# Kernel optimization log

Measured on AMD Instinct MI355X. Metric: run time of the kernel, lower is better.

Reference implementation:

```python
import jax, jax.numpy as jnp
import numpy as np

B, S, N = 1, 512, 256
C_M, C_Z, C_OPM, C_H, H = 64, 128, 32, 32, 8
INF = 1.0e6


def layer_norm(x, w, b, eps=1e-5):
    mu = x.mean(-1, keepdims=True)
    var = x.var(-1, keepdims=True)
    return (x - mu) / jnp.sqrt(var + eps) * w + b


def setup_inputs() -> dict:
    key = jax.random.key(0)
    ks = jax.random.split(key, 12)
    inp = {
        'm': jax.random.normal(ks[0], (B, S, N, C_M), jnp.float32),
        'z': jax.random.normal(ks[1], (B, N, N, C_Z), jnp.float32),
        'msa_mask': jnp.ones((B, S, N), jnp.float32),
        'pair_mask': jnp.ones((B, N, N), jnp.float32),
        # OuterProductMean params
        'opm_norm_w': jnp.ones((C_M,), jnp.float32),
        'opm_norm_b': jnp.zeros((C_M,), jnp.float32),
        'opm_a_w': jax.random.normal(ks[2], (C_OPM, C_M), jnp.float32) * 0.05,
        'opm_b_w': jax.random.normal(ks[3], (C_OPM, C_M), jnp.float32) * 0.05,
        'opm_o_w': jax.random.normal(ks[4], (C_Z, C_OPM * C_OPM), jnp.float32) * 0.02,
        'opm_o_b': jnp.zeros((C_Z,), jnp.float32),
        # PairWeightedAveraging params
        'pwa_norm_m_w': jnp.ones((C_M,), jnp.float32),
        'pwa_norm_m_b': jnp.zeros((C_M,), jnp.float32),
        'pwa_norm_z_w': jnp.ones((C_Z,), jnp.float32),
        'pwa_norm_z_b': jnp.zeros((C_Z,), jnp.float32),
        'pwa_m_w': jax.random.normal(ks[5], (H * C_H, C_M), jnp.float32) * 0.05,
        'pwa_g_w': jax.random.normal(ks[6], (H * C_H, C_M), jnp.float32) * 0.05,
        'pwa_z_w': jax.random.normal(ks[7], (H, C_Z), jnp.float32) * 0.05,
        'pwa_o_w': jax.random.normal(ks[8], (C_M, H * C_H), jnp.float32) * 0.02,
    }
    return inp


def reference(m, z, msa_mask, pair_mask,
              opm_norm_w, opm_norm_b, opm_a_w, opm_b_w, opm_o_w, opm_o_b,
              pwa_norm_m_w, pwa_norm_m_b, pwa_norm_z_w, pwa_norm_z_b,
              pwa_m_w, pwa_g_w, pwa_z_w, pwa_o_w):
    # ---- OuterProductMean: m (B,S,N,c_in), msa_mask (B,S,N) -> (B,N,N,c_z)
    mn = layer_norm(m, opm_norm_w, opm_norm_b)
    a = jnp.einsum('bsni,ci->bsnc', mn, opm_a_w) * msa_mask[..., None]  # (B,S,N,c)
    bb = jnp.einsum('bsni,ci->bsnc', mn, opm_b_w) * msa_mask[..., None]
    num_mask = jnp.clip(jnp.einsum('bsi,bsj->bij', msa_mask, msa_mask), 1.0)
    # outer product mean over S; flatten (c,d) with c-major to match torch reshape
    zt = jnp.einsum('bsic,bsjd->bijcd', a, bb).reshape(B, N, N, C_OPM * C_OPM)
    zt = zt / num_mask[..., None]
    z_opm = zt @ opm_o_w.T + opm_o_b  # (B,N,N,c_z)
    z_new = z + z_opm

    # ---- PairWeightedAveraging: m (B,S,N,c_m), z_new (B,N,N,c_z) -> (B,S,N,c_m)
    mn2 = layer_norm(m, pwa_norm_m_w, pwa_norm_m_b)
    zn = layer_norm(z_new, pwa_norm_z_w, pwa_norm_z_b)
    v = (mn2 @ pwa_m_w.T).reshape(B, S, N, H, C_H)            # (B,S,N,H,ch)
    bias = jnp.einsum('bijz,hz->bhij', zn, pwa_z_w)            # (B,H,N,N)
    bias = bias + (1.0 - pair_mask[:, None]) * (-INF)
    w = jax.nn.softmax(bias, axis=-1)
    g = jax.nn.sigmoid(mn2 @ pwa_g_w.T)                        # (B,S,N,H*ch)
    o = jnp.einsum('bhij,bsjhc->bsihc', w, v).reshape(B, S, N, H * C_H)
    out = (g * o) @ pwa_o_w.T                                  # (B,S,N,c_m)
    return out
```

## Files before the change

kernel.cpp:

```cpp
#include <hip/hip_runtime.h>
#include <stdint.h>

using u16 = unsigned short;
using u32 = unsigned int;

#define S_DIM 512
#define N_DIM 256
#define CM 64
#define CZ 128
#define NH 8
#define NPOS (S_DIM*N_DIM)
#define NPAIR (N_DIM*N_DIM)
#define CHS 256
#define CHPOS (CHS*N_DIM)

__device__ __forceinline__ float b2f(u16 h){ u32 u = ((u32)h)<<16; float f; __builtin_memcpy(&f,&u,4); return f; }
__device__ __forceinline__ u16 f2b(float f){ u32 u; __builtin_memcpy(&u,&f,4); u32 r = (u + 0x7fffu + ((u>>16)&1u))>>16; return (u16)r; }

typedef __bf16 bf16_t;
typedef bf16_t bf16x8 __attribute__((ext_vector_type(8)));
typedef float  f32x4  __attribute__((ext_vector_type(4)));

typedef const __attribute__((address_space(1))) void* gvp;
typedef __attribute__((address_space(3))) void* lvp;
#define GLOAD_LDS16(g, l) __builtin_amdgcn_global_load_lds((gvp)(uintptr_t)(g), (lvp)(uintptr_t)(l), 16, 0, 0)

__device__ __forceinline__ uint4 bfmul8(uint4 a, uint4 b){
  union{uint4 v; u16 h[8];} x,y,r;
  x.v=a; y.v=b;
  #pragma unroll
  for (int k=0;k<8;k++) r.h[k] = f2b(b2f(x.h[k])*b2f(y.h[k]));
  return r.v;
}

struct EpiArgs {
  const float* rowscale;
  u16*  out_b;
  float* out_f;
  int ldc;
};

constexpr int EPI_PLAIN=0, EPI_ROWSCALE=1, EPI_SIGMOID=2, EPI_VT=3, EPI_O=6;

template<int BM,int BN,int WR,int WC,int FM,int FN,int EPI,bool MULA=false>
__global__ __launch_bounds__(256) void gemm_k(const u16* __restrict__ A, const u16* __restrict__ A2,
                                              const u16* __restrict__ W,
                                              int K, size_t sAz, size_t sWz, EpiArgs ea)
{
  static_assert(BM==WR*FM*16 && BN==WC*FN*16 && WR*WC==4, "geom");
  __shared__ __align__(16) u16 lsA[BM*64];
  __shared__ __align__(16) u16 lsW[BN*64];
  const int tid  = threadIdx.x;
  const int lane = tid & 63;
  const int wv   = tid >> 6;
  const int wr   = wv / WC;
  const int wc   = wv % WC;
  const int m0   = blockIdx.y * BM;
  const int n0   = blockIdx.x * BN;
  const u16* Ab  = A  + (size_t)blockIdx.z * sAz + (size_t)m0 * K;
  const u16* A2b = MULA ? (A2 + (size_t)blockIdx.z * sAz + (size_t)m0 * K) : nullptr;
  const u16* Wb  = W  + (size_t)blockIdx.z * sWz + (size_t)n0 * K;

  f32x4 acc[FM][FN];
  #pragma unroll
  for (int i=0;i<FM;i++)
    #pragma unroll
    for (int j=0;j<FN;j++) acc[i][j] = (f32x4){0.f,0.f,0.f,0.f};

  const int nkt = K >> 6;
  for (int kt = 0; kt < nkt; ++kt) {
    if constexpr (!MULA) {
      #pragma unroll
      for (int c0 = 0; c0 < BM*8; c0 += 256) {
        int cc = c0 + (wv<<6) + lane;
        int row = cc>>3, kc = cc&7;
        GLOAD_LDS16(Ab + (size_t)row*K + (kt<<6) + ((kc ^ (row&7))<<3),
                    lsA + (size_t)(c0 + (wv<<6))*8);
      }
      #pragma unroll
      for (int c0 = 0; c0 < BN*8; c0 += 256) {
        int cc = c0 + (wv<<6) + lane;
        int row = cc>>3, kc = cc&7;
        GLOAD_LDS16(Wb + (size_t)row*K + (kt<<6) + ((kc ^ (row&7))<<3),
                    lsW + (size_t)(c0 + (wv<<6))*8);
      }
    } else {
      for (int c = tid; c < (BM+BN)*8; c += 256) {
        if (c < BM*8) {
          int row = c>>3, kc = c&7;
          size_t off = (size_t)row*K + (kt<<6) + (kc<<3);
          uint4 v = *reinterpret_cast<const uint4*>(Ab + off);
          uint4 v2 = *reinterpret_cast<const uint4*>(A2b + off);
          v = bfmul8(v, v2);
          *reinterpret_cast<uint4*>((char*)lsA + row*128 + ((kc<<4) ^ ((row&7)<<4))) = v;
        } else {
          int c2 = c - BM*8; int row = c2>>3, kc = c2&7;
          uint4 v = *reinterpret_cast<const uint4*>(Wb + (size_t)row*K + (kt<<6) + (kc<<3));
          *reinterpret_cast<uint4*>((char*)lsW + row*128 + ((kc<<4) ^ ((row&7)<<4))) = v;
        }
      }
    }
    __syncthreads();
    #pragma unroll
    for (int kk=0; kk<2; ++kk) {
      const int kb = (kk<<6) + ((lane>>4)<<4);
      bf16x8 af[FM], wf[FN];
      #pragma unroll
      for (int mf=0;mf<FM;mf++){
        int row = wr*FM*16 + mf*16 + (lane&15);
        af[mf] = *reinterpret_cast<const bf16x8*>((char*)lsA + row*128 + (kb ^ ((row&7)<<4)));
      }
      #pragma unroll
      for (int nf=0;nf<FN;nf++){
        int row = wc*FN*16 + nf*16 + (lane&15);
        wf[nf] = *reinterpret_cast<const bf16x8*>((char*)lsW + row*128 + (kb ^ ((row&7)<<4)));
      }
      #pragma unroll
      for (int mf=0;mf<FM;mf++)
        #pragma unroll
        for (int nf=0;nf<FN;nf++)
          acc[mf][nf] = __builtin_amdgcn_mfma_f32_16x16x32_bf16(af[mf], wf[nf], acc[mf][nf], 0,0,0);
    }
    __syncthreads();
  }

  const int hz = blockIdx.z;
  #pragma unroll
  for (int mf=0;mf<FM;mf++){
    #pragma unroll
    for (int nf=0;nf<FN;nf++){
      f32x4 v = acc[mf][nf];
      int col   = n0 + wc*FN*16 + nf*16 + (lane&15);
      int rbase = m0 + wr*FM*16 + mf*16 + ((lane>>4)<<2);
      #pragma unroll
      for (int r=0;r<4;r++){
        int row = rbase + r;
        float x = v[r];
        if constexpr (EPI==EPI_PLAIN) {
          ea.out_f[(size_t)row*ea.ldc + col] = x;
        } else if constexpr (EPI==EPI_ROWSCALE) {
          x *= ea.rowscale[row];
          ea.out_b[(size_t)row*ea.ldc + col] = f2b(x);
        } else if constexpr (EPI==EPI_SIGMOID) {
          x = 1.f/(1.f+__expf(-x));
          ea.out_b[(size_t)row*ea.ldc + col] = f2b(x);
        } else if constexpr (EPI==EPI_VT) {
          int hh = col>>5, cc = col&31, sl = row>>8, j = row&255;
          ea.out_b[((size_t)(hh*(CHS*32) + sl*32 + cc))*N_DIM + j] = f2b(x);
        } else if constexpr (EPI==EPI_O) {
          int sl = col>>5, cc = col&31;
          ea.out_b[(size_t)(sl*N_DIM + row)*256 + hz*32 + cc] = f2b(x);
        }
      }
    }
  }
}

__global__ __launch_bounds__(256,1) void opm_fused(const u16* __restrict__ a_t, const u16* __restrict__ b_t,
                                                   const float* __restrict__ recip, const u16* __restrict__ owp,
                                                   const float* __restrict__ obias, const float* __restrict__ z,
                                                   float* __restrict__ z_new)
{
  __shared__ __align__(16) u16 ls[16384];
  __shared__ __align__(16) u16 zt[16384];
  const int tid = threadIdx.x, lane = tid&63, wv = tid>>6;
  const int wr = wv>>1, wc = wv&1;
  const int bid = blockIdx.x;
  const int swz = (bid&7)*512 + (bid>>3);
  const int by = swz>>6, bx = swz&63;
  const u16* Ab = a_t + (size_t)by*128*S_DIM;
  const u16* Wb = b_t + (size_t)bx*128*S_DIM;
  u16* lsA = ls;
  u16* lsW = ls + 8192;

  f32x4 acc[4][4];
  #pragma unroll
  for (int i=0;i<4;i++)
    #pragma unroll
    for (int j=0;j<4;j++) acc[i][j] = (f32x4){0.f,0.f,0.f,0.f};

  for (int kt = 0; kt < 8; ++kt) {
    #pragma unroll
    for (int c0 = 0; c0 < 1024; c0 += 256) {
      int cc = c0 + (wv<<6) + lane;
      int row = cc>>3, kc = cc&7;
      size_t srcoff = (size_t)row*S_DIM + (kt<<6) + ((kc ^ (row&7))<<3);
      GLOAD_LDS16(Ab + srcoff, lsA + (size_t)(c0 + (wv<<6))*8);
      GLOAD_LDS16(Wb + srcoff, lsW + (size_t)(c0 + (wv<<6))*8);
    }
    __syncthreads();
    #pragma unroll
    for (int kk=0; kk<2; ++kk) {
      const int kb = (kk<<6) + ((lane>>4)<<4);
      bf16x8 af[4], wf[4];
      #pragma unroll
      for (int mf=0;mf<4;mf++){
        int row = wr*64 + mf*16 + (lane&15);
        af[mf] = *reinterpret_cast<const bf16x8*>((char*)lsA + row*128 + (kb ^ ((row&7)<<4)));
      }
      #pragma unroll
      for (int nf=0;nf<4;nf++){
        int row = wc*64 + nf*16 + (lane&15);
        wf[nf] = *reinterpret_cast<const bf16x8*>((char*)lsW + row*128 + (kb ^ ((row&7)<<4)));
      }
      #pragma unroll
      for (int mf=0;mf<4;mf++)
        #pragma unroll
        for (int nf=0;nf<4;nf++)
          acc[mf][nf] = __builtin_amdgcn_mfma_f32_16x16x32_bf16(af[mf], wf[nf], acc[mf][nf], 0,0,0);
    }
    __syncthreads();
  }

  #pragma unroll
  for (int mf=0;mf<4;mf++){
    #pragma unroll
    for (int nf=0;nf<4;nf++){
      int ii = 2*wr + (mf>>1);
      int jj = 2*wc + (nf>>1);
      int p  = ii*4 + jj;
      int d  = ((nf&1)<<4) + (lane&15);
      int c0 = ((mf&1)<<4) + ((lane>>4)<<2);
      float rv = recip[(by*4+ii)*N_DIM + bx*4 + jj];
      f32x4 v = acc[mf][nf];
      union { uint2 u; u16 h[4]; } pk;
      #pragma unroll
      for (int r=0;r<4;r++) pk.h[r] = f2b(v[r]*rv);
      int byte = p*2048 + (((d + p)&31)<<6) + ((c0*2) ^ (((d>>1)&3)<<4));
      *reinterpret_cast<uint2*>((char*)zt + byte) = pk.u;
    }
  }
  __syncthreads();

  f32x4 acc2[2] = {(f32x4){0,0,0,0},(f32x4){0,0,0,0}};
  u16* lsw2 = ls + wv*4096;
  const u16* owpw = owp + wv*4096;
  for (int it=0; it<8; ++it){
    #pragma unroll
    for (int j=0;j<8;j++)
      GLOAD_LDS16(owpw + (size_t)it*16384 + j*512 + lane*8, lsw2 + j*512);
    asm volatile("s_waitcnt vmcnt(0)" ::: "memory");
    __builtin_amdgcn_sched_barrier(0);
    #pragma unroll
    for (int kk=0; kk<4; ++kk){
      int d = it*4 + kk;
      int p  = lane&15;
      int c0 = (lane>>4)<<3;
      bf16x8 af = *reinterpret_cast<const bf16x8*>((char*)zt + p*2048 + (((d + p)&31)<<6) +
                    ((c0*2) ^ (((d>>1)&3)<<4)));
      const int kb = (kk<<6) + ((lane>>4)<<4);
      #pragma unroll
      for (int nf=0;nf<2;nf++){
        int rl = nf*16 + (lane&15);
        bf16x8 wf = *reinterpret_cast<const bf16x8*>((char*)lsw2 + rl*256 + (kb ^ ((rl&7)<<4)));
        acc2[nf] = __builtin_amdgcn_mfma_f32_16x16x32_bf16(af, wf, acc2[nf], 0,0,0);
      }
    }
    __builtin_amdgcn_sched_barrier(0);
  }

  #pragma unroll
  for (int nf=0;nf<2;nf++){
    int col = wv*32 + nf*16 + (lane&15);
    #pragma unroll
    for (int r=0;r<4;r++){
      int p = ((lane>>4)<<2) + r;
      size_t gp = (size_t)(by*4 + (p>>2))*N_DIM + bx*4 + (p&3);
      z_new[gp*CZ + col] = acc2[nf][r] + obias[col] + z[gp*CZ + col];
    }
  }
}

__global__ __launch_bounds__(256) void ln_m_kernel(const float* __restrict__ m, const float* ow, const float* ob,
                                                   const float* pw, const float* pb,
                                                   u16* __restrict__ mo, u16* __restrict__ mp)
{
  int row  = blockIdx.x*4 + (threadIdx.x>>6);
  int lane = threadIdx.x & 63;
  float x = m[(size_t)row*CM + lane];
  float s = x, s2 = x*x;
  #pragma unroll
  for (int off=32; off; off>>=1){ s += __shfl_xor(s,off); s2 += __shfl_xor(s2,off); }
  float mu   = s*(1.f/64.f);
  float var  = s2*(1.f/64.f) - mu*mu;
  float rstd = rsqrtf(var + 1e-5f);
  float mn = (x-mu)*rstd;
  mo[(size_t)row*CM+lane] = f2b(mn*ow[lane] + ob[lane]);
  mp[(size_t)row*CM+lane] = f2b(mn*pw[lane] + pb[lane]);
}

__global__ __launch_bounds__(256) void cvt_w_kernel(const float* __restrict__ aw, const float* __restrict__ bw,
                                                    const float* __restrict__ ow, const float* __restrict__ mw,
                                                    const float* __restrict__ gw, const float* __restrict__ o2w,
                                                    u16* __restrict__ wb)
{
  int e = blockIdx.x*256 + threadIdx.x;
  float v;
  if (e < 4096)        { int r = e>>6, c = e&63; v = (r<32)? aw[r*64+c] : bw[(r-32)*64+c]; }
  else if (e < 135168) { int t = e-4096; int it = t>>14, rem = t&16383, row = rem>>7, h = rem&127;
                         int kl = h ^ ((row&7)<<3);
                         int kp = it*128 + kl;
                         int d = kp>>5, c = kp&31;
                         v = ow[row*1024 + c*32 + d]; }
  else if (e < 151552) { v = mw[e-135168]; }
  else if (e < 167936) { v = gw[e-151552]; }
  else                 { v = o2w[e-167936]; }
  wb[e] = f2b(v);
}

__global__ __launch_bounds__(256) void transpose_ab_kernel(const u16* __restrict__ ab,
                                                           u16* __restrict__ a_t, u16* __restrict__ b_t)
{
  __shared__ u16 t[64][72];
  int sb = blockIdx.x, i = blockIdx.y, tid = threadIdx.x;
  for (int c = tid; c < 512; c += 256){
    int sl = c>>3, kc = c&7;
    union { uint4 v; u16 h[8]; } u;
    u.v = *reinterpret_cast<const uint4*>(ab + ((size_t)(sb*64+sl)*N_DIM + i)*64 + (kc<<3));
    #pragma unroll
    for (int k=0;k<8;k++) t[sl][kc*8+k] = u.h[k];
  }
  __syncthreads();
  for (int c = tid; c < 512; c += 256){
    int cc = c>>3, sc = c&7;
    union { uint4 v; u16 h[8]; } u;
    #pragma unroll
    for (int k=0;k<8;k++) u.h[k] = t[sc*8+k][cc];
    u16* dst = (cc < 32) ? (a_t + (size_t)(i*32+cc)*S_DIM) : (b_t + (size_t)(i*32+cc-32)*S_DIM);
    *reinterpret_cast<uint4*>(dst + sb*64 + (sc<<3)) = u.v;
  }
}

__global__ __launch_bounds__(256) void num_mask_kernel(const float* __restrict__ msa, float* __restrict__ recip){
  int i = blockIdx.x, j = threadIdx.x;
  float s = 0.f;
  #pragma unroll 8
  for (int t=0;t<S_DIM;t++) s += msa[t*N_DIM+i] * msa[t*N_DIM+j];
  recip[i*N_DIM + j] = 1.f / fmaxf(s, 1.f);
}

__global__ __launch_bounds__(256) void ln_bias_kernel(const float* __restrict__ z_new, const float* zw, const float* zb,
                                                      const float* zwh, const float* pm, float* __restrict__ bias)
{
  int p    = blockIdx.x*4 + (threadIdx.x>>6);
  int lane = threadIdx.x & 63;
  const float* zr = z_new + (size_t)p*CZ;
  float x0 = zr[lane*2], x1 = zr[lane*2+1];
  float s = x0+x1, s2 = x0*x0 + x1*x1;
  #pragma unroll
  for (int off=32; off; off>>=1){ s += __shfl_xor(s,off); s2 += __shfl_xor(s2,off); }
  float mu   = s*(1.f/128.f);
  float var  = s2*(1.f/128.f) - mu*mu;
  float rstd = rsqrtf(var + 1e-5f);
  float zn0 = (x0-mu)*rstd*zw[lane*2]   + zb[lane*2];
  float zn1 = (x1-mu)*rstd*zw[lane*2+1] + zb[lane*2+1];
  float bm = (1.f - pm[p]) * (-1.0e6f);
  float outv = 0.f;
  #pragma unroll
  for (int hh=0; hh<8; hh++){
    float tp = zn0*zwh[hh*CZ + lane*2] + zn1*zwh[hh*CZ + lane*2+1];
    #pragma unroll
    for (int off=32; off; off>>=1) tp += __shfl_xor(tp,off);
    if (lane == hh) outv = tp + bm;
  }
  if (lane < 8) bias[(size_t)lane*NPAIR + p] = outv;
}

__global__ __launch_bounds__(256) void softmax_kernel(const float* __restrict__ bias, u16* __restrict__ w_sm){
  int r    = blockIdx.x*4 + (threadIdx.x>>6);
  int lane = threadIdx.x & 63;
  const float* src = bias + (size_t)(r>>8)*NPAIR + (size_t)(r&255)*N_DIM;
  float4 xv = *reinterpret_cast<const float4*>(src + lane*4);
  float mx = fmaxf(fmaxf(xv.x,xv.y), fmaxf(xv.z,xv.w));
  #pragma unroll
  for (int off=32; off; off>>=1) mx = fmaxf(mx, __shfl_xor(mx,off));
  float e0 = __expf(xv.x-mx), e1 = __expf(xv.y-mx), e2 = __expf(xv.z-mx), e3 = __expf(xv.w-mx);
  float s = e0+e1+e2+e3;
  #pragma unroll
  for (int off=32; off; off>>=1) s += __shfl_xor(s,off);
  float rs = 1.f/s;
  ushort4 st; st.x=f2b(e0*rs); st.y=f2b(e1*rs); st.z=f2b(e2*rs); st.w=f2b(e3*rs);
  *reinterpret_cast<ushort4*>(w_sm + (size_t)r*N_DIM + lane*4) = st;
}

extern "C" void kernel_launch(void* const* d_in, const int* in_sizes, int n_in,
                              void* d_out, int out_size, void* d_ws, size_t ws_size,
                              hipStream_t stream)
{
  const float* m      = (const float*)d_in[0];
  const float* z      = (const float*)d_in[1];
  const float* msa    = (const float*)d_in[2];
  const float* pmask  = (const float*)d_in[3];
  const float* opm_nw = (const float*)d_in[4];
  const float* opm_nb = (const float*)d_in[5];
  const float* opm_aw = (const float*)d_in[6];
  const float* opm_bw = (const float*)d_in[7];
  const float* opm_ow = (const float*)d_in[8];
  const float* opm_ob = (const float*)d_in[9];
  const float* pwa_nmw= (const float*)d_in[10];
  const float* pwa_nmb= (const float*)d_in[11];
  const float* pwa_nzw= (const float*)d_in[12];
  const float* pwa_nzb= (const float*)d_in[13];
  const float* pwa_mw = (const float*)d_in[14];
  const float* pwa_gw = (const float*)d_in[15];
  const float* pwa_zw = (const float*)d_in[16];
  const float* pwa_ow = (const float*)d_in[17];
  float* out = (float*)d_out;
  char* ws = (char*)d_ws;

  const size_t MB = 1024*1024;
  u16*  mn_pwa = (u16*)(ws + 0);
  u16*  mn_opm = (u16*)(ws + 16*MB);
  u16*  ab     = (u16*)(ws + 32*MB);
  u16*  a_t    = (u16*)(ws + 48*MB);
  u16*  b_t    = (u16*)(ws + 56*MB);
  float* z_new = (float*)(ws + 64*MB);
  float* bias  = (float*)(ws + 128*MB);
  u16*  w_sm   = (u16*)(ws + 130*MB);
  float* recip = (float*)(ws + 131*MB);
  u16*  wb     = (u16*)(ws + 131*MB + 512*1024);
  u16*  v_t  = (u16*)(ws + 16*MB);
  u16*  gbuf = (u16*)(ws + 48*MB);
  u16*  obuf = (u16*)(ws + 80*MB);

  const u16* w_ab = wb;
  const u16* owp  = wb + 4096;
  const u16* mw_b = wb + 135168;
  const u16* gw_b = wb + 151552;
  const u16* ow_b = wb + 167936;

  ln_m_kernel<<<dim3(NPOS/4),256,0,stream>>>(m, opm_nw, opm_nb, pwa_nmw, pwa_nmb, mn_opm, mn_pwa);
  cvt_w_kernel<<<dim3(184320/256),256,0,stream>>>(opm_aw, opm_bw, opm_ow, pwa_mw, pwa_gw, pwa_ow, wb);
  { EpiArgs ea{}; ea.rowscale = msa; ea.out_b = ab; ea.ldc = 64;
    gemm_k<128,64,2,2,4,2,EPI_ROWSCALE><<<dim3(1,NPOS/128),256,0,stream>>>(mn_opm, nullptr, w_ab, 64, 0,0, ea); }
  transpose_ab_kernel<<<dim3(8,256),256,0,stream>>>(ab, a_t, b_t);
  num_mask_kernel<<<dim3(256),256,0,stream>>>(msa, recip);
  opm_fused<<<dim3(4096),256,0,stream>>>(a_t, b_t, recip, owp, opm_ob, z, z_new);
  ln_bias_kernel<<<dim3(NPAIR/4),256,0,stream>>>(z_new, pwa_nzw, pwa_nzb, pwa_zw, pmask, bias);
  softmax_kernel<<<dim3(2048/4),256,0,stream>>>(bias, w_sm);

  for (int sc=0; sc<2; ++sc){
    const u16* mnp = mn_pwa + (size_t)sc*CHPOS*CM;
    { EpiArgs ea{}; ea.out_b = v_t;
      gemm_k<128,128,2,2,4,4,EPI_VT><<<dim3(2,CHPOS/128),256,0,stream>>>(mnp, nullptr, mw_b, 64, 0,0, ea); }
    { EpiArgs ea{}; ea.out_b = gbuf; ea.ldc = 256;
      gemm_k<128,128,2,2,4,4,EPI_SIGMOID><<<dim3(2,CHPOS/128),256,0,stream>>>(mnp, nullptr, gw_b, 64, 0,0, ea); }
    { EpiArgs ea{}; ea.out_b = obuf;
      gemm_k<128,128,2,2,4,4,EPI_O><<<dim3((CHS*32)/128, 2, NH),256,0,stream>>>(w_sm, nullptr, v_t, 256,
            (size_t)NPAIR, (size_t)(CHS*32)*N_DIM, ea); }
    { EpiArgs ea{}; ea.out_f = out + (size_t)sc*CHPOS*CM; ea.ldc = 64;
      gemm_k<128,64,2,2,4,2,EPI_PLAIN,true><<<dim3(1,CHPOS/128),256,0,stream>>>(gbuf, obuf, ow_b, 256, 0,0, ea); }
  }
}
```

Before: 529.4 us.

## Stage VT epilogue through LDS for coalesced stores and shrink OPM LDS footprint

The VT-transpose GEMM epilogue now writes accumulators into a swizzled shared-memory tile and then emits 16-byte coalesced global stores, replacing scattered 2-byte stores into the transposed layout. The fused outer-product-mean kernel merges its two LDS arrays into one smaller buffer, reuses the first-stage region for the zt tile, and streams the output-projection weights in half-sized chunks over twice as many iterations. The weight pre-packing kernel is changed to match. Its block-to-tile mapping is also reworked so that each XCD covers a contiguous 2D region. This adds an extra barrier in the epilogue and more load/wait steps in the OPM second stage, in exchange for lower LDS use and better store coalescing and cache locality.

```diff
diff --git a/kernel.cpp b/kernel.cpp
--- a/kernel.cpp
+++ b/kernel.cpp
@@ -48,8 +48,9 @@
                                               int K, size_t sAz, size_t sWz, EpiArgs ea)
 {
   static_assert(BM==WR*FM*16 && BN==WC*FN*16 && WR*WC==4, "geom");
-  __shared__ __align__(16) u16 lsA[BM*64];
-  __shared__ __align__(16) u16 lsW[BN*64];
+  __shared__ __align__(16) u16 ls[(BM+BN)*64];
+  u16* lsA = ls;
+  u16* lsW = ls + BM*64;
   const int tid  = threadIdx.x;
   const int lane = tid & 63;
   const int wv   = tid >> 6;
@@ -124,32 +125,55 @@
     __syncthreads();
   }
 
-  const int hz = blockIdx.z;
-  #pragma unroll
-  for (int mf=0;mf<FM;mf++){
-    #pragma unroll
-    for (int nf=0;nf<FN;nf++){
-      f32x4 v = acc[mf][nf];
-      int col   = n0 + wc*FN*16 + nf*16 + (lane&15);
-      int rbase = m0 + wr*FM*16 + mf*16 + ((lane>>4)<<2);
-      #pragma unroll
-      for (int r=0;r<4;r++){
-        int row = rbase + r;
-        float x = v[r];
-        if constexpr (EPI==EPI_PLAIN) {
-          ea.out_f[(size_t)row*ea.ldc + col] = x;
-        } else if constexpr (EPI==EPI_ROWSCALE) {
-          x *= ea.rowscale[row];
-          ea.out_b[(size_t)row*ea.ldc + col] = f2b(x);
-        } else if constexpr (EPI==EPI_SIGMOID) {
-          x = 1.f/(1.f+__expf(-x));
-          ea.out_b[(size_t)row*ea.ldc + col] = f2b(x);
-        } else if constexpr (EPI==EPI_VT) {
-          int hh = col>>5, cc = col&31, sl = row>>8, j = row&255;
-          ea.out_b[((size_t)(hh*(CHS*32) + sl*32 + cc))*N_DIM + j] = f2b(x);
-        } else if constexpr (EPI==EPI_O) {
-          int sl = col>>5, cc = col&31;
-          ea.out_b[(size_t)(sl*N_DIM + row)*256 + hz*32 + cc] = f2b(x);
+  if constexpr (EPI==EPI_VT) {
+    #pragma unroll
+    for (int mf=0;mf<FM;mf++){
+      #pragma unroll
+      for (int nf=0;nf<FN;nf++){
+        f32x4 v = acc[mf][nf];
+        int hcrow = wc*FN*16 + nf*16 + (lane&15);
+        int jl0   = wr*FM*16 + mf*16 + ((lane>>4)<<2);
+        union { uint2 u; u16 h[4]; } pk;
+        #pragma unroll
+        for (int r=0;r<4;r++) pk.h[r] = f2b(v[r]);
+        *reinterpret_cast<uint2*>((char*)ls + hcrow*256 + ((jl0*2) ^ ((hcrow&7)<<4))) = pk.u;
+      }
+    }
+    __syncthreads();
+    const int sl = m0>>8, j0 = m0&255, hb = n0>>5;
+    #pragma unroll
+    for (int itc=0; itc<8; ++itc){
+      int idx = itc*256 + tid;
+      int hcrow = idx>>4, q = idx&15;
+      uint4 vv = *reinterpret_cast<const uint4*>((char*)ls + hcrow*256 + ((q*16) ^ ((hcrow&7)<<4)));
+      int dstrow = (hb + (hcrow>>5))*(CHS*32) + sl*32 + (hcrow&31);
+      *reinterpret_cast<uint4*>(ea.out_b + (size_t)dstrow*N_DIM + j0 + q*8) = vv;
+    }
+  } else {
+    const int hz = blockIdx.z;
+    #pragma unroll
+    for (int mf=0;mf<FM;mf++){
+      #pragma unroll
+      for (int nf=0;nf<FN;nf++){
+        f32x4 v = acc[mf][nf];
+        int col   = n0 + wc*FN*16 + nf*16 + (lane&15);
+        int rbase = m0 + wr*FM*16 + mf*16 + ((lane>>4)<<2);
+        #pragma unroll
+        for (int r=0;r<4;r++){
+          int row = rbase + r;
+          float x = v[r];
+          if constexpr (EPI==EPI_PLAIN) {
+            ea.out_f[(size_t)row*ea.ldc + col] = x;
+          } else if constexpr (EPI==EPI_ROWSCALE) {
+            x *= ea.rowscale[row];
+            ea.out_b[(size_t)row*ea.ldc + col] = f2b(x);
+          } else if constexpr (EPI==EPI_SIGMOID) {
+            x = 1.f/(1.f+__expf(-x));
+            ea.out_b[(size_t)row*ea.ldc + col] = f2b(x);
+          } else if constexpr (EPI==EPI_O) {
+            int sl2 = col>>5, cc = col&31;
+            ea.out_b[(size_t)(sl2*N_DIM + row)*256 + hz*32 + cc] = f2b(x);
+          }
         }
       }
     }
@@ -161,13 +185,13 @@
                                                    const float* __restrict__ obias, const float* __restrict__ z,
                                                    float* __restrict__ z_new)
 {
-  __shared__ __align__(16) u16 ls[16384];
-  __shared__ __align__(16) u16 zt[16384];
+  __shared__ __align__(16) u16 ls[24576];
   const int tid = threadIdx.x, lane = tid&63, wv = tid>>6;
   const int wr = wv>>1, wc = wv&1;
   const int bid = blockIdx.x;
-  const int swz = (bid&7)*512 + (bid>>3);
-  const int by = swz>>6, bx = swz&63;
+  const int xcd = bid&7, l = bid>>3;
+  const int by = ((xcd>>1)<<4) + (l&15);
+  const int bx = ((xcd&1)<<5) + (l>>4);
   const u16* Ab = a_t + (size_t)by*128*S_DIM;
   const u16* Wb = b_t + (size_t)bx*128*S_DIM;
   u16* lsA = ls;
@@ -227,32 +251,32 @@
       #pragma unroll
       for (int r=0;r<4;r++) pk.h[r] = f2b(v[r]*rv);
       int byte = p*2048 + (((d + p)&31)<<6) + ((c0*2) ^ (((d>>1)&3)<<4));
-      *reinterpret_cast<uint2*>((char*)zt + byte) = pk.u;
+      *reinterpret_cast<uint2*>((char*)ls + byte) = pk.u;
     }
   }
   __syncthreads();
 
   f32x4 acc2[2] = {(f32x4){0,0,0,0},(f32x4){0,0,0,0}};
-  u16* lsw2 = ls + wv*4096;
-  const u16* owpw = owp + wv*4096;
-  for (int it=0; it<8; ++it){
-    #pragma unroll
-    for (int j=0;j<8;j++)
-      GLOAD_LDS16(owpw + (size_t)it*16384 + j*512 + lane*8, lsw2 + j*512);
+  u16* lsw2 = ls + 16384 + wv*2048;
+  const u16* owpw = owp + wv*2048;
+  for (int it=0; it<16; ++it){
+    #pragma unroll
+    for (int j=0;j<4;j++)
+      GLOAD_LDS16(owpw + (size_t)it*8192 + j*512 + lane*8, lsw2 + j*512);
     asm volatile("s_waitcnt vmcnt(0)" ::: "memory");
     __builtin_amdgcn_sched_barrier(0);
     #pragma unroll
-    for (int kk=0; kk<4; ++kk){
-      int d = it*4 + kk;
+    for (int kk=0; kk<2; ++kk){
+      int d = it*2 + kk;
       int p  = lane&15;
       int c0 = (lane>>4)<<3;
-      bf16x8 af = *reinterpret_cast<const bf16x8*>((char*)zt + p*2048 + (((d + p)&31)<<6) +
+      bf16x8 af = *reinterpret_cast<const bf16x8*>((char*)ls + p*2048 + (((d + p)&31)<<6) +
                     ((c0*2) ^ (((d>>1)&3)<<4)));
       const int kb = (kk<<6) + ((lane>>4)<<4);
       #pragma unroll
       for (int nf=0;nf<2;nf++){
         int rl = nf*16 + (lane&15);
-        bf16x8 wf = *reinterpret_cast<const bf16x8*>((char*)lsw2 + rl*256 + (kb ^ ((rl&7)<<4)));
+        bf16x8 wf = *reinterpret_cast<const bf16x8*>((char*)lsw2 + rl*128 + (kb ^ ((rl&7)<<4)));
         acc2[nf] = __builtin_amdgcn_mfma_f32_16x16x32_bf16(af, wf, acc2[nf], 0,0,0);
       }
     }
@@ -297,9 +321,9 @@
   int e = blockIdx.x*256 + threadIdx.x;
   float v;
   if (e < 4096)        { int r = e>>6, c = e&63; v = (r<32)? aw[r*64+c] : bw[(r-32)*64+c]; }
-  else if (e < 135168) { int t = e-4096; int it = t>>14, rem = t&16383, row = rem>>7, h = rem&127;
+  else if (e < 135168) { int t = e-4096; int it = t>>13, rem = t&8191, row = rem>>6, h = rem&63;
                          int kl = h ^ ((row&7)<<3);
-                         int kp = it*128 + kl;
+                         int kp = it*64 + kl;
                          int d = kp>>5, c = kp&31;
                          v = ow[row*1024 + c*32 + d]; }
   else if (e < 151552) { v = mw[e-135168]; }
```

New measurement: 523.5 us. No clear change (-1.1%).
